# Kernel tuning notes

Hardware: AMD Instinct MI355X
Metric: run time of the kernel (lower is better)

## Reference

```python
import jax, jax.numpy as jnp
import numpy as np

K = 8  # init kwarg k

def setup_inputs() -> dict:
    key = jax.random.key(0)
    x = jax.random.normal(key, (4096, 50257), dtype=jnp.float32)
    return {"x": x}

def reference(x):
    # torch.topk(x, k) along last dim -> (values, indices), sorted descending
    top_values, top_indices = jax.lax.top_k(x, K)
    return (top_values, top_indices)
```

## Files before the change

kernel.cpp:

```cpp
#include <hip/hip_runtime.h>
#include <cfloat>
#include <cstdint>

#define K 8
#define NT 256
#define NW (NT / 64)
#define WARM 4
#define CH2 16

typedef float f32x4 __attribute__((ext_vector_type(4)));

__global__ __launch_bounds__(NT) void topk8_kernel(const float* __restrict__ x,
                                                   float* __restrict__ out,
                                                   int ncols, int nrows) {
    const int row  = blockIdx.x;
    const int tid  = threadIdx.x;
    const int lane = tid & 63;
    const int wave = tid >> 6;
    const float* __restrict__ rowp = x + (size_t)row * (size_t)ncols;

    __shared__ float sw[NW * K];
    __shared__ float sv[NW];
    __shared__ int   si[NW];
    __shared__ int   st[NW];
    __shared__ float rv[K];
    __shared__ int   ri[K];

    float v[K];
    int   id[K];
#pragma unroll
    for (int i = 0; i < K; ++i) { v[i] = -FLT_MAX; id[i] = 0x7fffffff; }

    auto insert = [&](float val, int idx) {
        if (val > v[K - 1]) {
            v[K - 1] = val; id[K - 1] = idx;
#pragma unroll
            for (int p = K - 1; p > 0; --p) {
                if (v[p] > v[p - 1]) {
                    float tv = v[p]; v[p] = v[p - 1]; v[p - 1] = tv;
                    int   ti = id[p]; id[p] = id[p - 1]; id[p - 1] = ti;
                }
            }
        }
    };

    auto refresh = [&](float Told) -> float {
        float t0 = v[0], t1 = v[1], t2 = v[2], t3 = v[3];
        float t4 = v[4], t5 = v[5], t6 = v[6], t7 = v[7];
#pragma unroll
        for (int r = 0; r < K; ++r) {
            float m = t0;
#pragma unroll
            for (int off = 32; off >= 1; off >>= 1)
                m = fmaxf(m, __shfl_xor(m, off));
            const bool pop = (t0 == m);
            t0 = pop ? t1 : t0;
            t1 = pop ? t2 : t1;
            t2 = pop ? t3 : t2;
            t3 = pop ? t4 : t3;
            t4 = pop ? t5 : t4;
            t5 = pop ? t6 : t5;
            t6 = pop ? t7 : t6;
            t7 = pop ? -FLT_MAX : t7;
            if (lane == 0) sw[wave * K + r] = m;
        }
        __syncthreads();
        float g0 = -FLT_MAX, g1 = -FLT_MAX, g2 = -FLT_MAX, g3 = -FLT_MAX;
        float g4 = -FLT_MAX, g5 = -FLT_MAX, g6 = -FLT_MAX, g7 = -FLT_MAX;
#pragma unroll
        for (int i = 0; i < NW * K; ++i) {
            const float xx = sw[i];
            g7 = __builtin_amdgcn_fmed3f(g6, g7, xx);
            g6 = __builtin_amdgcn_fmed3f(g5, g6, xx);
            g5 = __builtin_amdgcn_fmed3f(g4, g5, xx);
            g4 = __builtin_amdgcn_fmed3f(g3, g4, xx);
            g3 = __builtin_amdgcn_fmed3f(g2, g3, xx);
            g2 = __builtin_amdgcn_fmed3f(g1, g2, xx);
            g1 = __builtin_amdgcn_fmed3f(g0, g1, xx);
            g0 = fmaxf(g0, xx);
        }
        __syncthreads();
        return fmaxf(Told, g7);
    };

    const int mis  = (int)(((uintptr_t)rowp >> 2) & 3);
    int head = (4 - mis) & 3;
    if (head > ncols) head = ncols;
    if (tid < head) insert(rowp[tid], tid);

    const int nvec4 = (ncols - head) >> 2;
    const f32x4* __restrict__ vp = (const f32x4*)(rowp + head);

    int j = tid;

    for (int w = 0; w < WARM; ++w, j += NT) {
        if (j < nvec4) {
            f32x4 f = vp[j];
            const int b = head + 4 * j;
            insert(f[0], b); insert(f[1], b + 1); insert(f[2], b + 2); insert(f[3], b + 3);
        }
    }

    float T = refresh(-FLT_MAX);

    for (int w = 0; w < CH2; ++w, j += NT) {
        if (j < nvec4) {
            f32x4 f = vp[j];
            const float m = fmaxf(fmaxf(f[0], f[1]), fmaxf(f[2], f[3]));
            if (m >= T) {
                const int b = head + 4 * j;
                if (f[0] >= T) insert(f[0], b);
                if (f[1] >= T) insert(f[1], b + 1);
                if (f[2] >= T) insert(f[2], b + 2);
                if (f[3] >= T) insert(f[3], b + 3);
            }
        }
    }

    T = refresh(T);

    for (; j + 3 * NT < nvec4; j += 4 * NT) {
        f32x4 f0 = __builtin_nontemporal_load(vp + j);
        f32x4 f1 = __builtin_nontemporal_load(vp + j + NT);
        f32x4 f2 = __builtin_nontemporal_load(vp + j + 2 * NT);
        f32x4 f3 = __builtin_nontemporal_load(vp + j + 3 * NT);
        const float m0 = fmaxf(fmaxf(f0[0], f0[1]), fmaxf(f0[2], f0[3]));
        const float m1 = fmaxf(fmaxf(f1[0], f1[1]), fmaxf(f1[2], f1[3]));
        const float m2 = fmaxf(fmaxf(f2[0], f2[1]), fmaxf(f2[2], f2[3]));
        const float m3 = fmaxf(fmaxf(f3[0], f3[1]), fmaxf(f3[2], f3[3]));
        const float mm = fmaxf(fmaxf(m0, m1), fmaxf(m2, m3));
        if (mm >= T) {
            if (m0 >= T) {
                const int b = head + 4 * j;
                if (f0[0] >= T) insert(f0[0], b);
                if (f0[1] >= T) insert(f0[1], b + 1);
                if (f0[2] >= T) insert(f0[2], b + 2);
                if (f0[3] >= T) insert(f0[3], b + 3);
            }
            if (m1 >= T) {
                const int b = head + 4 * (j + NT);
                if (f1[0] >= T) insert(f1[0], b);
                if (f1[1] >= T) insert(f1[1], b + 1);
                if (f1[2] >= T) insert(f1[2], b + 2);
                if (f1[3] >= T) insert(f1[3], b + 3);
            }
            if (m2 >= T) {
                const int b = head + 4 * (j + 2 * NT);
                if (f2[0] >= T) insert(f2[0], b);
                if (f2[1] >= T) insert(f2[1], b + 1);
                if (f2[2] >= T) insert(f2[2], b + 2);
                if (f2[3] >= T) insert(f2[3], b + 3);
            }
            if (m3 >= T) {
                const int b = head + 4 * (j + 3 * NT);
                if (f3[0] >= T) insert(f3[0], b);
                if (f3[1] >= T) insert(f3[1], b + 1);
                if (f3[2] >= T) insert(f3[2], b + 2);
                if (f3[3] >= T) insert(f3[3], b + 3);
            }
        }
    }
    for (; j < nvec4; j += NT) {
        f32x4 f = vp[j];
        const float m = fmaxf(fmaxf(f[0], f[1]), fmaxf(f[2], f[3]));
        if (m >= T) {
            const int b = head + 4 * j;
            if (f[0] >= T) insert(f[0], b);
            if (f[1] >= T) insert(f[1], b + 1);
            if (f[2] >= T) insert(f[2], b + 2);
            if (f[3] >= T) insert(f[3], b + 3);
        }
    }

    const int tb = head + 4 * nvec4;
    for (int c = tb + tid; c < ncols; c += NT) insert(rowp[c], c);

    for (int r = 0; r < K; ++r) {
        float bv = v[0];
        int   bi = id[0];
        int   bt = tid;
#pragma unroll
        for (int off = 32; off >= 1; off >>= 1) {
            float ov = __shfl_xor(bv, off);
            int   oi = __shfl_xor(bi, off);
            int   ot = __shfl_xor(bt, off);
            if (ov > bv || (ov == bv && oi < bi)) { bv = ov; bi = oi; bt = ot; }
        }
        if (lane == 0) { sv[wave] = bv; si[wave] = bi; st[wave] = bt; }
        __syncthreads();

        float wv = sv[0]; int wi = si[0]; int wt = st[0];
#pragma unroll
        for (int w = 1; w < NW; ++w) {
            if (sv[w] > wv || (sv[w] == wv && si[w] < wi)) {
                wv = sv[w]; wi = si[w]; wt = st[w];
            }
        }

        if (tid == wt) {
#pragma unroll
            for (int p = 0; p < K - 1; ++p) { v[p] = v[p + 1]; id[p] = id[p + 1]; }
            v[K - 1] = -FLT_MAX; id[K - 1] = 0x7fffffff;
        }
        if (tid == 0) { rv[r] = wv; ri[r] = wi; }
        __syncthreads();
    }

    if (tid < K) {
        out[(size_t)row * K + tid]                     = rv[tid];
        out[(size_t)nrows * K + (size_t)row * K + tid] = (float)ri[tid];
    }
}

extern "C" void kernel_launch(void* const* d_in, const int* in_sizes, int n_in,
                              void* d_out, int out_size, void* d_ws, size_t ws_size,
                              hipStream_t stream) {
    const float* x = (const float*)d_in[0];
    float* out = (float*)d_out;
    const int nrows = 4096;
    const int ncols = in_sizes[0] / nrows;
    topk8_kernel<<<nrows, NT, 0, stream>>>(x, out, ncols, nrows);
}
```

Measured before the change: 147.8 us.

## Replace block-wide final top-k merge with per-wave select plus single-wave merge

The final selection now has each wave pick its own top 8 with lane-local shuffles, then one wave merges the 32 candidates, which removes 16 block barriers from the final merge. The warm-up and second phase are restructured into 4-wide vectorized chunks that reuse a gated lambda and nontemporal loads. The risk is extra per-lane work in the final wave-only merge, and the warm-up batch now has a slightly different size and ordering.

```diff
diff --git a/kernel.cpp b/kernel.cpp
--- a/kernel.cpp
+++ b/kernel.cpp
@@ -5,8 +5,7 @@
 #define K 8
 #define NT 256
 #define NW (NT / 64)
-#define WARM 4
-#define CH2 16
+#define CH2B 4
 
 typedef float f32x4 __attribute__((ext_vector_type(4)));
 
@@ -19,12 +18,8 @@
     const int wave = tid >> 6;
     const float* __restrict__ rowp = x + (size_t)row * (size_t)ncols;
 
-    __shared__ float sw[NW * K];
-    __shared__ float sv[NW];
-    __shared__ int   si[NW];
-    __shared__ int   st[NW];
-    __shared__ float rv[K];
-    __shared__ int   ri[K];
+    __shared__ float swv[NW * K];
+    __shared__ int   swi[NW * K];
 
     float v[K];
     int   id[K];
@@ -62,14 +57,14 @@
             t5 = pop ? t6 : t5;
             t6 = pop ? t7 : t6;
             t7 = pop ? -FLT_MAX : t7;
-            if (lane == 0) sw[wave * K + r] = m;
+            if (lane == 0) swv[wave * K + r] = m;
         }
         __syncthreads();
         float g0 = -FLT_MAX, g1 = -FLT_MAX, g2 = -FLT_MAX, g3 = -FLT_MAX;
         float g4 = -FLT_MAX, g5 = -FLT_MAX, g6 = -FLT_MAX, g7 = -FLT_MAX;
 #pragma unroll
         for (int i = 0; i < NW * K; ++i) {
-            const float xx = sw[i];
+            const float xx = swv[i];
             g7 = __builtin_amdgcn_fmed3f(g6, g7, xx);
             g6 = __builtin_amdgcn_fmed3f(g5, g6, xx);
             g5 = __builtin_amdgcn_fmed3f(g4, g5, xx);
@@ -93,37 +88,12 @@
 
     int j = tid;
 
-    for (int w = 0; w < WARM; ++w, j += NT) {
-        if (j < nvec4) {
-            f32x4 f = vp[j];
-            const int b = head + 4 * j;
-            insert(f[0], b); insert(f[1], b + 1); insert(f[2], b + 2); insert(f[3], b + 3);
-        }
-    }
-
-    float T = refresh(-FLT_MAX);
-
-    for (int w = 0; w < CH2; ++w, j += NT) {
-        if (j < nvec4) {
-            f32x4 f = vp[j];
-            const float m = fmaxf(fmaxf(f[0], f[1]), fmaxf(f[2], f[3]));
-            if (m >= T) {
-                const int b = head + 4 * j;
-                if (f[0] >= T) insert(f[0], b);
-                if (f[1] >= T) insert(f[1], b + 1);
-                if (f[2] >= T) insert(f[2], b + 2);
-                if (f[3] >= T) insert(f[3], b + 3);
-            }
-        }
-    }
-
-    T = refresh(T);
-
-    for (; j + 3 * NT < nvec4; j += 4 * NT) {
-        f32x4 f0 = __builtin_nontemporal_load(vp + j);
-        f32x4 f1 = __builtin_nontemporal_load(vp + j + NT);
-        f32x4 f2 = __builtin_nontemporal_load(vp + j + 2 * NT);
-        f32x4 f3 = __builtin_nontemporal_load(vp + j + 3 * NT);
+    float T = -FLT_MAX;
+    auto gated4 = [&](int jj) {
+        f32x4 f0 = __builtin_nontemporal_load(vp + jj);
+        f32x4 f1 = __builtin_nontemporal_load(vp + jj + NT);
+        f32x4 f2 = __builtin_nontemporal_load(vp + jj + 2 * NT);
+        f32x4 f3 = __builtin_nontemporal_load(vp + jj + 3 * NT);
         const float m0 = fmaxf(fmaxf(f0[0], f0[1]), fmaxf(f0[2], f0[3]));
         const float m1 = fmaxf(fmaxf(f1[0], f1[1]), fmaxf(f1[2], f1[3]));
         const float m2 = fmaxf(fmaxf(f2[0], f2[1]), fmaxf(f2[2], f2[3]));
@@ -131,35 +101,83 @@
         const float mm = fmaxf(fmaxf(m0, m1), fmaxf(m2, m3));
         if (mm >= T) {
             if (m0 >= T) {
-                const int b = head + 4 * j;
+                const int b = head + 4 * jj;
                 if (f0[0] >= T) insert(f0[0], b);
                 if (f0[1] >= T) insert(f0[1], b + 1);
                 if (f0[2] >= T) insert(f0[2], b + 2);
                 if (f0[3] >= T) insert(f0[3], b + 3);
             }
             if (m1 >= T) {
-                const int b = head + 4 * (j + NT);
+                const int b = head + 4 * (jj + NT);
                 if (f1[0] >= T) insert(f1[0], b);
                 if (f1[1] >= T) insert(f1[1], b + 1);
                 if (f1[2] >= T) insert(f1[2], b + 2);
                 if (f1[3] >= T) insert(f1[3], b + 3);
             }
             if (m2 >= T) {
-                const int b = head + 4 * (j + 2 * NT);
+                const int b = head + 4 * (jj + 2 * NT);
                 if (f2[0] >= T) insert(f2[0], b);
                 if (f2[1] >= T) insert(f2[1], b + 1);
                 if (f2[2] >= T) insert(f2[2], b + 2);
                 if (f2[3] >= T) insert(f2[3], b + 3);
             }
             if (m3 >= T) {
-                const int b = head + 4 * (j + 3 * NT);
+                const int b = head + 4 * (jj + 3 * NT);
                 if (f3[0] >= T) insert(f3[0], b);
                 if (f3[1] >= T) insert(f3[1], b + 1);
                 if (f3[2] >= T) insert(f3[2], b + 2);
                 if (f3[3] >= T) insert(f3[3], b + 3);
             }
         }
-    }
+    };
+
+    if (j + 3 * NT < nvec4) {
+        f32x4 f0 = __builtin_nontemporal_load(vp + j);
+        f32x4 f1 = __builtin_nontemporal_load(vp + j + NT);
+        f32x4 f2 = __builtin_nontemporal_load(vp + j + 2 * NT);
+        f32x4 f3 = __builtin_nontemporal_load(vp + j + 3 * NT);
+        int b = head + 4 * j;
+        insert(f0[0], b); insert(f0[1], b + 1); insert(f0[2], b + 2); insert(f0[3], b + 3);
+        b = head + 4 * (j + NT);
+        insert(f1[0], b); insert(f1[1], b + 1); insert(f1[2], b + 2); insert(f1[3], b + 3);
+        b = head + 4 * (j + 2 * NT);
+        insert(f2[0], b); insert(f2[1], b + 1); insert(f2[2], b + 2); insert(f2[3], b + 3);
+        b = head + 4 * (j + 3 * NT);
+        insert(f3[0], b); insert(f3[1], b + 1); insert(f3[2], b + 2); insert(f3[3], b + 3);
+        j += 4 * NT;
+    } else {
+        for (int w = 0; w < 4 && j < nvec4; ++w, j += NT) {
+            f32x4 f = vp[j];
+            const int b = head + 4 * j;
+            insert(f[0], b); insert(f[1], b + 1); insert(f[2], b + 2); insert(f[3], b + 3);
+        }
+    }
+
+    T = refresh(-FLT_MAX);
+
+    for (int bk = 0; bk < CH2B; ++bk) {
+        if (j + 3 * NT < nvec4) {
+            gated4(j);
+            j += 4 * NT;
+        } else {
+            for (int w = 0; w < 4 && j < nvec4; ++w, j += NT) {
+                f32x4 f = vp[j];
+                const float m = fmaxf(fmaxf(f[0], f[1]), fmaxf(f[2], f[3]));
+                if (m >= T) {
+                    const int b = head + 4 * j;
+                    if (f[0] >= T) insert(f[0], b);
+                    if (f[1] >= T) insert(f[1], b + 1);
+                    if (f[2] >= T) insert(f[2], b + 2);
+                    if (f[3] >= T) insert(f[3], b + 3);
+                }
+            }
+        }
+    }
+
+    T = refresh(T);
+
+    for (; j + 3 * NT < nvec4; j += 4 * NT) gated4(j);
+
     for (; j < nvec4; j += NT) {
         f32x4 f = vp[j];
         const float m = fmaxf(fmaxf(f[0], f[1]), fmaxf(f[2], f[3]));
@@ -175,10 +193,11 @@
     const int tb = head + 4 * nvec4;
     for (int c = tb + tid; c < ncols; c += NT) insert(rowp[c], c);
 
+#pragma unroll
     for (int r = 0; r < K; ++r) {
         float bv = v[0];
         int   bi = id[0];
-        int   bt = tid;
+        int   bt = lane;
 #pragma unroll
         for (int off = 32; off >= 1; off >>= 1) {
             float ov = __shfl_xor(bv, off);
@@ -186,29 +205,36 @@
             int   ot = __shfl_xor(bt, off);
             if (ov > bv || (ov == bv && oi < bi)) { bv = ov; bi = oi; bt = ot; }
         }
-        if (lane == 0) { sv[wave] = bv; si[wave] = bi; st[wave] = bt; }
-        __syncthreads();
-
-        float wv = sv[0]; int wi = si[0]; int wt = st[0];
-#pragma unroll
-        for (int w = 1; w < NW; ++w) {
-            if (sv[w] > wv || (sv[w] == wv && si[w] < wi)) {
-                wv = sv[w]; wi = si[w]; wt = st[w];
-            }
-        }
-
-        if (tid == wt) {
+        if (lane == bt) {
 #pragma unroll
             for (int p = 0; p < K - 1; ++p) { v[p] = v[p + 1]; id[p] = id[p + 1]; }
             v[K - 1] = -FLT_MAX; id[K - 1] = 0x7fffffff;
         }
-        if (tid == 0) { rv[r] = wv; ri[r] = wi; }
-        __syncthreads();
-    }
-
-    if (tid < K) {
-        out[(size_t)row * K + tid]                     = rv[tid];
-        out[(size_t)nrows * K + (size_t)row * K + tid] = (float)ri[tid];
+        if (lane == 0) { swv[wave * K + r] = bv; swi[wave * K + r] = bi; }
+    }
+    __syncthreads();
+
+    if (wave == 0) {
+        float cv = (lane < NW * K) ? swv[lane] : -FLT_MAX;
+        int   ci = (lane < NW * K) ? swi[lane] : 0x7fffffff;
+#pragma unroll
+        for (int r = 0; r < K; ++r) {
+            float bv = cv;
+            int   bi = ci;
+            int   bt = lane;
+#pragma unroll
+            for (int off = 32; off >= 1; off >>= 1) {
+                float ov = __shfl_xor(bv, off);
+                int   oi = __shfl_xor(bi, off);
+                int   ot = __shfl_xor(bt, off);
+                if (ov > bv || (ov == bv && oi < bi)) { bv = ov; bi = oi; bt = ot; }
+            }
+            if (lane == bt) { cv = -FLT_MAX; ci = 0x7fffffff; }
+            if (lane == 0) {
+                out[(size_t)row * K + r]                     = bv;
+                out[(size_t)nrows * K + (size_t)row * K + r] = (float)bi;
+            }
+        }
     }
 }
 
```

New measurement: 147.9 us. Within noise of the previous version (+0.1%).
